# Optimization experiments

Measured on AMD Instinct MI355X. Metric: run time of the kernel, lower is better.

## Reference

```python
import jax, jax.numpy as jnp
import numpy as np

HIDDEN = 1024
HEADS = 16
HEAD_DIM = HIDDEN // HEADS  # 64
B, S = 2, 2048


def setup_inputs() -> dict:
    key = jax.random.key(0)
    ks = jax.random.split(key, 12)
    lim_h = 1.0 / np.sqrt(HEAD_DIM)
    lim_o = 1.0 / np.sqrt(HIDDEN)
    u = lambda k, shape, lim: jax.random.uniform(k, shape, jnp.float32, -lim, lim)
    return {
        "query": jax.random.normal(ks[0], (B, S, HIDDEN), jnp.float32),
        "key": jax.random.normal(ks[1], (B, S, HIDDEN), jnp.float32),
        "value": jax.random.normal(ks[2], (B, S, HIDDEN), jnp.float32),
        "mask": jax.random.randint(ks[3], (B, 1, S, S), 0, 2, jnp.int32),
        "Wq": u(ks[4], (HEAD_DIM, HEAD_DIM), lim_h), "bq": u(ks[5], (HEAD_DIM,), lim_h),
        "Wk": u(ks[6], (HEAD_DIM, HEAD_DIM), lim_h), "bk": u(ks[7], (HEAD_DIM,), lim_h),
        "Wv": u(ks[8], (HEAD_DIM, HEAD_DIM), lim_h), "bv": u(ks[9], (HEAD_DIM,), lim_h),
        "Wo": u(ks[10], (HIDDEN, HIDDEN), lim_o), "bo": u(ks[11], (HIDDEN,), lim_o),
    }


def reference(query, key, value, mask, Wq, bq, Wk, bk, Wv, bv, Wo, bo):
    b = query.shape[0]
    # view [B, S, H, D]; per-head linear is SHARED across heads (head_dim x head_dim)
    q = query.reshape(b, -1, HEADS, HEAD_DIM) @ Wq.T + bq
    k = key.reshape(b, -1, HEADS, HEAD_DIM) @ Wk.T + bk
    v = value.reshape(b, -1, HEADS, HEAD_DIM) @ Wv.T + bv
    scores = jnp.einsum('nqhd,nkhd->nhqk', q, k)  # [B, H, Sq, Sk]
    scores = jnp.where(mask == 0, jnp.float32(-1e20), scores)
    # NOTE: original scales by sqrt(hidden_dim), not sqrt(head_dim)
    attn = jax.nn.softmax(scores / np.sqrt(HIDDEN).astype(np.float32), axis=3)
    out = jnp.einsum('nhql,nlhd->nqhd', attn, v).reshape(b, query.shape[1], HIDDEN)
    return out @ Wo.T + bo
```

## Files before the change

kernel.cpp:

```cpp
#include <hip/hip_runtime.h>
#include <hip/hip_bf16.h>

#define NB 2
#define NS 2048
#define NH 16
#define ND 64
#define NHID 1024

#define QSCALE 0.045084220f

typedef __attribute__((ext_vector_type(8))) short bf16x8;
typedef __attribute__((ext_vector_type(4))) short s16x4;
typedef __attribute__((ext_vector_type(4))) float f32x4;

typedef __attribute__((address_space(3))) unsigned int lds_u32;
typedef __attribute__((address_space(1))) unsigned int glb_u32;

__device__ inline void gl_lds16(const void* g, void* l) {
  __builtin_amdgcn_global_load_lds((const glb_u32*)g, (lds_u32*)l, 16, 0, 0);
}

__device__ inline short f2bf(float f) {
  __hip_bfloat16 h = __float2bfloat16(f);
  short s; __builtin_memcpy(&s, &h, 2); return s;
}

__device__ inline bf16x8 cvt8(const float* __restrict__ p) {
  float4 x = *(const float4*)p;
  float4 y = *(const float4*)(p + 4);
  bf16x8 r;
  r[0] = f2bf(x.x); r[1] = f2bf(x.y); r[2] = f2bf(x.z); r[3] = f2bf(x.w);
  r[4] = f2bf(y.x); r[5] = f2bf(y.y); r[6] = f2bf(y.z); r[7] = f2bf(y.w);
  return r;
}

__global__ __launch_bounds__(256) void prep(
    const int* __restrict__ mask, unsigned* __restrict__ mp,
    const float* __restrict__ Wq, const float* __restrict__ Wk,
    const float* __restrict__ Wv, const float* __restrict__ Wo,
    short* __restrict__ Wq_b, short* __restrict__ Wk_b,
    short* __restrict__ Wv_b, short* __restrict__ Wo_b)
{
  if (blockIdx.x < 1024) {
    int idx = blockIdx.x * 256 + threadIdx.x;
    const int4* src = (const int4*)(mask + (long)idx * 32);
    unsigned w = 0;
#pragma unroll
    for (int i = 0; i < 8; ++i) {
      int4 v = src[i];
      w |= (v.x != 0 ? 1u : 0u) << (i * 4 + 0);
      w |= (v.y != 0 ? 1u : 0u) << (i * 4 + 1);
      w |= (v.z != 0 ? 1u : 0u) << (i * 4 + 2);
      w |= (v.w != 0 ? 1u : 0u) << (i * 4 + 3);
    }
    mp[idx] = w;
  } else {
    int i = ((blockIdx.x - 1024) * 256 + threadIdx.x) * 4;
    const float* src; short* dst; int off; float sc = 1.0f;
    if (i < 1048576)      { src = Wo; dst = Wo_b; off = i; }
    else {
      int j = i - 1048576;
      if (j < 4096)       { src = Wq; dst = Wq_b; off = j; sc = QSCALE; }
      else if (j < 8192)  { src = Wk; dst = Wk_b; off = j - 4096; }
      else                { src = Wv; dst = Wv_b; off = j - 8192; }
    }
    float4 v = *(const float4*)(src + off);
    s16x4 o;
    o[0] = f2bf(v.x * sc); o[1] = f2bf(v.y * sc);
    o[2] = f2bf(v.z * sc); o[3] = f2bf(v.w * sc);
    *(s16x4*)(dst + off) = o;
  }
}

__global__ __launch_bounds__(256) void qk_proj(
    const float* __restrict__ qin, const float* __restrict__ kin,
    const short* __restrict__ Wq_b, const float* __restrict__ bq,
    const short* __restrict__ Wk_b, const float* __restrict__ bk,
    short* __restrict__ Qws, short* __restrict__ Kws)
{
  __shared__ __align__(16) short ldsT[4][16][72];
  const int tid = threadIdx.x;
  const int w = tid >> 6, lane = tid & 63;
  const int c = lane & 15, qq = lane >> 4;
  const int t = blockIdx.x * 4 + w;
  const int b = t >> 11, s = t & (NS - 1);
  const int aoff = (t * 16 + c) * 64 + qq * 8;
  const int row0 = lane >> 3, inner = lane & 7;

#pragma unroll
  for (int m = 0; m < 2; ++m) {
    const float* X  = (m == 0) ? qin  : kin;
    const short* W  = (m == 0) ? Wq_b : Wk_b;
    const float* bb = (m == 0) ? bq   : bk;
    short* dst      = (m == 0) ? Qws  : Kws;
    const float bsc = (m == 0) ? QSCALE : 1.0f;

    bf16x8 a0 = cvt8(X + aoff);
    bf16x8 a1 = cvt8(X + aoff + 32);

#pragma unroll
    for (int nt = 0; nt < 4; ++nt) {
      f32x4 z = {0.f, 0.f, 0.f, 0.f};
      const short* wp = W + (nt * 16 + c) * 64 + qq * 8;
      bf16x8 b0 = *(const bf16x8*)(wp);
      bf16x8 b1 = *(const bf16x8*)(wp + 32);
      z = __builtin_amdgcn_mfma_f32_16x16x32_bf16(a0, b0, z, 0, 0, 0);
      z = __builtin_amdgcn_mfma_f32_16x16x32_bf16(a1, b1, z, 0, 0, 0);
      float bias = bb[nt * 16 + c] * bsc;
#pragma unroll
      for (int r = 0; r < 4; ++r)
        ldsT[w][qq * 4 + r][nt * 16 + c] = f2bf(z[r] + bias);
    }

    bf16x8 v0 = *(const bf16x8*)&ldsT[w][row0][inner * 8];
    bf16x8 v1 = *(const bf16x8*)&ldsT[w][row0 + 8][inner * 8];
    int bh0 = b * NH + row0, bh1 = b * NH + row0 + 8;
    *(bf16x8*)(dst + (bh0 * NS + s) * 64 + inner * 8) = v0;
    *(bf16x8*)(dst + (bh1 * NS + s) * 64 + inner * 8) = v1;
  }
}

__global__ __launch_bounds__(256) void vproj(
    const float* __restrict__ vin, const short* __restrict__ Wv_b,
    const float* __restrict__ bv, short* __restrict__ Vt)
{
  __shared__ __align__(16) short ldsVT[64][72];
  const int tid = threadIdx.x;
  const int g = tid >> 6, lane = tid & 63;
  const int c = lane & 15, qq = lane >> 4;
  const int bh = blockIdx.x >> 5;
  const int stile = blockIdx.x & 31;
  const int b = bh >> 4, h = bh & 15;
  const int sb = stile * 64;

  bf16x8 wv[8];
  float bias[4];
#pragma unroll
  for (int nt = 0; nt < 4; ++nt) {
    const short* wp = Wv_b + (nt * 16 + c) * 64 + qq * 8;
    wv[nt * 2]     = *(const bf16x8*)(wp);
    wv[nt * 2 + 1] = *(const bf16x8*)(wp + 32);
    bias[nt] = bv[nt * 16 + c];
  }

  const float* ap = vin + ((size_t)((b * NS + sb + 16 * g + c) * 16 + h)) * 64 + qq * 8;
  bf16x8 a0 = cvt8(ap);
  bf16x8 a1 = cvt8(ap + 32);
#pragma unroll
  for (int nt = 0; nt < 4; ++nt) {
    f32x4 z = {0.f, 0.f, 0.f, 0.f};
    z = __builtin_amdgcn_mfma_f32_16x16x32_bf16(a0, wv[nt * 2], z, 0, 0, 0);
    z = __builtin_amdgcn_mfma_f32_16x16x32_bf16(a1, wv[nt * 2 + 1], z, 0, 0, 0);
    ushort4 u;
    u.x = (unsigned short)f2bf(z[0] + bias[nt]);
    u.y = (unsigned short)f2bf(z[1] + bias[nt]);
    u.z = (unsigned short)f2bf(z[2] + bias[nt]);
    u.w = (unsigned short)f2bf(z[3] + bias[nt]);
    *(ushort4*)&ldsVT[nt * 16 + c][16 * g + qq * 4] = u;
  }
  __syncthreads();

#pragma unroll
  for (int j = 0; j < 2; ++j) {
    int idx = tid + 256 * j;
    int d = idx >> 3, unit = idx & 7;
    bf16x8 o = *(const bf16x8*)&ldsVT[d][unit * 8];
    *(bf16x8*)(Vt + ((size_t)(bh * 64 + d)) * NS + sb + unit * 8) = o;
  }
}

__global__ __launch_bounds__(256) void attn(
    const short* __restrict__ Qws, const short* __restrict__ Kws,
    const short* __restrict__ Vt, const unsigned* __restrict__ Mp,
    short* __restrict__ AO)
{
  __shared__ __align__(16) short Ks[2][64][64];
  __shared__ __align__(16) short Vs[2][64][64];
  __shared__ __align__(16) short Ps[4][32][72];

  const int tid = threadIdx.x;
  const int w = tid >> 6, lane = tid & 63;
  const int c = lane & 15, qq = lane >> 4;
  const int bh = blockIdx.x & 31;
  const int qtile = blockIdx.x >> 5;
  const int b = bh >> 4, h = bh & 15;
  const int qbase = qtile * 128 + w * 32;

  const short* Qp = Qws + (size_t)bh * (NS * 64);
  const short* Kp = Kws + (size_t)bh * (NS * 64);
  const short* Vp = Vt + (size_t)bh * (64 * NS);
  const unsigned* mrow = Mp + (size_t)b * (NS * (NS / 32));

  bf16x8 aq[2][2];
#pragma unroll
  for (int nq = 0; nq < 2; ++nq) {
    const short* qp = Qp + (qbase + nq * 16 + c) * 64 + qq * 8;
    aq[nq][0] = *(const bf16x8*)(qp);
    aq[nq][1] = *(const bf16x8*)(qp + 32);
  }

  float lsum[2] = {0.f, 0.f};
  f32x4 O[2][4];
#pragma unroll
  for (int nq = 0; nq < 2; ++nq)
#pragma unroll
    for (int dt = 0; dt < 4; ++dt) { f32x4 z = {0.f, 0.f, 0.f, 0.f}; O[nq][dt] = z; }

  const int srow = lane >> 3;
  const int sunit = (lane & 7) ^ srow;
  auto stage = [&](int kt, int buf) {
#pragma unroll
    for (int i = 0; i < 2; ++i) {
      int j = w * 2 + i;
      const short* gk = Kp + ((size_t)(kt * 64 + j * 8 + srow)) * 64 + sunit * 8;
      gl_lds16(gk, &Ks[buf][0][0] + j * 512);
      const short* gv = Vp + ((size_t)(j * 8 + srow)) * NS + kt * 64 + sunit * 8;
      gl_lds16(gv, &Vs[buf][0][0] + j * 512);
    }
  };

  stage(0, 0);
  __syncthreads();

  for (int kt = 0; kt < NS / 64; ++kt) {
    const int buf = kt & 1;
    if (kt < NS / 64 - 1) stage(kt + 1, buf ^ 1);

    uint2 mw[2];
#pragma unroll
    for (int nq = 0; nq < 2; ++nq)
      mw[nq] = *(const uint2*)(mrow +
          (size_t)(qbase + nq * 16 + c) * (NS / 32) + kt * 2);

    f32x4 st[4][2];
#pragma unroll
    for (int mt = 0; mt < 4; ++mt) {
      const short* kb = &Ks[buf][mt * 16 + c][0];
      bf16x8 ak0 = *(const bf16x8*)(kb + ((qq ^ (c & 7)) << 3));
      bf16x8 ak1 = *(const bf16x8*)(kb + (((4 + qq) ^ (c & 7)) << 3));
#pragma unroll
      for (int nq = 0; nq < 2; ++nq) {
        f32x4 z = {0.f, 0.f, 0.f, 0.f};
        z = __builtin_amdgcn_mfma_f32_16x16x32_bf16(ak0, aq[nq][0], z, 0, 0, 0);
        z = __builtin_amdgcn_mfma_f32_16x16x32_bf16(ak1, aq[nq][1], z, 0, 0, 0);
        st[mt][nq] = z;
      }
    }

#pragma unroll
    for (int mt = 0; mt < 4; ++mt) {
#pragma unroll
      for (int nq = 0; nq < 2; ++nq) {
        unsigned wsel = (mt & 2) ? mw[nq].y : mw[nq].x;
        unsigned nib = (wsel >> (((mt & 1) << 4) + (qq << 2))) & 0xFu;
        f32x4 s = st[mt][nq];
        float e0 = (nib & 1u) ? __builtin_amdgcn_exp2f(s[0]) : 0.f;
        float e1 = (nib & 2u) ? __builtin_amdgcn_exp2f(s[1]) : 0.f;
        float e2 = (nib & 4u) ? __builtin_amdgcn_exp2f(s[2]) : 0.f;
        float e3 = (nib & 8u) ? __builtin_amdgcn_exp2f(s[3]) : 0.f;
        lsum[nq] += (e0 + e1) + (e2 + e3);
        ushort4 u;
        u.x = (unsigned short)f2bf(e0);
        u.y = (unsigned short)f2bf(e1);
        u.z = (unsigned short)f2bf(e2);
        u.w = (unsigned short)f2bf(e3);
        *(ushort4*)&Ps[w][nq * 16 + c][mt * 16 + (qq << 2)] = u;
      }
    }

#pragma unroll
    for (int ks = 0; ks < 2; ++ks) {
      bf16x8 pf[2];
#pragma unroll
      for (int nq = 0; nq < 2; ++nq)
        pf[nq] = *(const bf16x8*)&Ps[w][nq * 16 + c][ks * 32 + qq * 8];
#pragma unroll
      for (int dt = 0; dt < 4; ++dt) {
        const short* vb = &Vs[buf][dt * 16 + c][0];
        bf16x8 vf = *(const bf16x8*)(vb + ((((ks << 2) + qq) ^ (c & 7)) << 3));
#pragma unroll
        for (int nq = 0; nq < 2; ++nq)
          O[nq][dt] = __builtin_amdgcn_mfma_f32_16x16x32_bf16(vf, pf[nq], O[nq][dt], 0, 0, 0);
      }
    }

    __syncthreads();
  }

#pragma unroll
  for (int nq = 0; nq < 2; ++nq) {
    float v = lsum[nq];
    v += __shfl_xor(v, 16);
    v += __shfl_xor(v, 32);
    lsum[nq] = 1.0f / fmaxf(v, 1e-30f);
  }

#pragma unroll
  for (int nq = 0; nq < 2; ++nq) {
    int row = qbase + nq * 16 + c;
#pragma unroll
    for (int dt = 0; dt < 4; ++dt) {
      ushort4 u;
      u.x = (unsigned short)f2bf(O[nq][dt][0] * lsum[nq]);
      u.y = (unsigned short)f2bf(O[nq][dt][1] * lsum[nq]);
      u.z = (unsigned short)f2bf(O[nq][dt][2] * lsum[nq]);
      u.w = (unsigned short)f2bf(O[nq][dt][3] * lsum[nq]);
      *(ushort4*)(AO + ((size_t)(b * NS + row)) * NHID + h * 64 + dt * 16 + qq * 4) = u;
    }
  }
}

__global__ __launch_bounds__(256, 2) void oproj(
    const short* __restrict__ X, const short* __restrict__ Wo_b,
    const float* __restrict__ bo, float* __restrict__ out)
{
  __shared__ __align__(16) short As[2][64][64];
  __shared__ __align__(16) short Bs[2][128][64];
  const int tid = threadIdx.x;
  const int w = tid >> 6, lane = tid & 63;
  const int c = lane & 15, qq = lane >> 4;
  const int rowbase = blockIdx.x * 64;
  const int colbase = blockIdx.y * 128;
  const int mh = w & 1, nh = w >> 1;

  const int srow = lane >> 3;
  const int sunit = (lane & 7) ^ srow;

  auto stage = [&](int kb, int buf) {
#pragma unroll
    for (int i = 0; i < 6; ++i) {
      int t = w * 6 + i;
      if (t < 8) {
        const short* g = X + (size_t)(rowbase + t * 8 + srow) * NHID
                           + kb * 64 + sunit * 8;
        gl_lds16(g, &As[buf][0][0] + t * 512);
      } else {
        int j = t - 8;
        const short* g = Wo_b + (size_t)(colbase + j * 8 + srow) * NHID
                              + kb * 64 + sunit * 8;
        gl_lds16(g, &Bs[buf][0][0] + j * 512);
      }
    }
  };

  f32x4 acc[2][4];
#pragma unroll
  for (int mt = 0; mt < 2; ++mt)
#pragma unroll
    for (int nt = 0; nt < 4; ++nt) { f32x4 z = {0.f, 0.f, 0.f, 0.f}; acc[mt][nt] = z; }

  stage(0, 0);
  __syncthreads();

  for (int kb = 0; kb < NHID / 64; ++kb) {
    const int buf = kb & 1;
    if (kb < NHID / 64 - 1) stage(kb + 1, buf ^ 1);

    bf16x8 af[2][2];
#pragma unroll
    for (int mt = 0; mt < 2; ++mt) {
      const short* ap = &As[buf][mh * 32 + mt * 16 + c][0];
#pragma unroll
      for (int ks = 0; ks < 2; ++ks)
        af[mt][ks] = *(const bf16x8*)(ap + ((((ks << 2) + qq) ^ (c & 7)) << 3));
    }
#pragma unroll
    for (int nt = 0; nt < 4; ++nt) {
      const short* bp = &Bs[buf][nh * 64 + nt * 16 + c][0];
#pragma unroll
      for (int ks = 0; ks < 2; ++ks) {
        bf16x8 bf = *(const bf16x8*)(bp + ((((ks << 2) + qq) ^ (c & 7)) << 3));
#pragma unroll
        for (int mt = 0; mt < 2; ++mt)
          acc[mt][nt] = __builtin_amdgcn_mfma_f32_16x16x32_bf16(af[mt][ks], bf, acc[mt][nt], 0, 0, 0);
      }
    }

    __syncthreads();
  }

#pragma unroll
  for (int nt = 0; nt < 4; ++nt) {
    int col = colbase + nh * 64 + nt * 16 + c;
    float bias = bo[col];
#pragma unroll
    for (int mt = 0; mt < 2; ++mt) {
      int row = rowbase + mh * 32 + mt * 16 + qq * 4;
#pragma unroll
      for (int r = 0; r < 4; ++r)
        out[(size_t)(row + r) * NHID + col] = acc[mt][nt][r] + bias;
    }
  }
}

extern "C" void kernel_launch(void* const* d_in, const int* in_sizes, int n_in,
                              void* d_out, int out_size, void* d_ws, size_t ws_size,
                              hipStream_t stream) {
  const float* qin = (const float*)d_in[0];
  const float* kin = (const float*)d_in[1];
  const float* vin = (const float*)d_in[2];
  const int*  mask = (const int*)d_in[3];
  const float* Wq = (const float*)d_in[4];
  const float* bq = (const float*)d_in[5];
  const float* Wk = (const float*)d_in[6];
  const float* bk = (const float*)d_in[7];
  const float* Wv = (const float*)d_in[8];
  const float* bv = (const float*)d_in[9];
  const float* Wo = (const float*)d_in[10];
  const float* bo = (const float*)d_in[11];
  float* out = (float*)d_out;

  char* ws = (char*)d_ws;
  short* Qws = (short*)(ws);
  short* Kws = (short*)(ws + (size_t)(8 << 20));
  short* Vt  = (short*)(ws + (size_t)(16 << 20));
  short* AO  = (short*)(ws + (size_t)(24 << 20));
  unsigned* Mp = (unsigned*)(ws + (size_t)(32 << 20));
  short* Wo_b = (short*)(ws + (size_t)(33 << 20));
  short* Wq_b = (short*)(ws + (size_t)(35 << 20));
  short* Wk_b = (short*)(ws + (size_t)(35 << 20) + 8192);
  short* Wv_b = (short*)(ws + (size_t)(35 << 20) + 16384);

  prep<<<2060, 256, 0, stream>>>(mask, Mp, Wq, Wk, Wv, Wo, Wq_b, Wk_b, Wv_b, Wo_b);
  qk_proj<<<NB * NS / 4, 256, 0, stream>>>(qin, kin, Wq_b, bq, Wk_b, bk, Qws, Kws);
  vproj<<<(NB * NH) * (NS / 64), 256, 0, stream>>>(vin, Wv_b, bv, Vt);
  attn<<<(NB * NH) * (NS / 128), 256, 0, stream>>>(Qws, Kws, Vt, Mp, AO);
  oproj<<<dim3(64, 8), 256, 0, stream>>>(AO, Wo_b, bo, out);
}
```

Measured before the change: 222.3 us.

## Use two waves with 64 query rows each and MFMA-based row sums

The attention kernel now runs 128 threads per block, and each wave owns 64 query rows instead of 32. This doubles reuse of every K/V fragment read from LDS per MFMA and halves the number of waves issuing LDS reads. The softmax denominator is now computed by an extra MFMA of the bf16 P tile against a vector of ones, replacing the scalar adds and cross-lane shuffles. The cost is higher register pressure from 16 O accumulators plus 4 sum accumulators, fewer waves per block to hide latency, and row sums taken from bf16-rounded probabilities.

```diff
diff --git a/kernel.cpp b/kernel.cpp
--- a/kernel.cpp
+++ b/kernel.cpp
@@ -169,14 +169,14 @@
   }
 }
 
-__global__ __launch_bounds__(256) void attn(
+__global__ __launch_bounds__(128) void attn(
     const short* __restrict__ Qws, const short* __restrict__ Kws,
     const short* __restrict__ Vt, const unsigned* __restrict__ Mp,
     short* __restrict__ AO)
 {
   __shared__ __align__(16) short Ks[2][64][64];
   __shared__ __align__(16) short Vs[2][64][64];
-  __shared__ __align__(16) short Ps[4][32][72];
+  __shared__ __align__(16) short Ps[2][64][72];
 
   const int tid = threadIdx.x;
   const int w = tid >> 6, lane = tid & 63;
@@ -184,34 +184,41 @@
   const int bh = blockIdx.x & 31;
   const int qtile = blockIdx.x >> 5;
   const int b = bh >> 4, h = bh & 15;
-  const int qbase = qtile * 128 + w * 32;
+  const int qbase = qtile * 128 + w * 64;
 
   const short* Qp = Qws + (size_t)bh * (NS * 64);
   const short* Kp = Kws + (size_t)bh * (NS * 64);
   const short* Vp = Vt + (size_t)bh * (64 * NS);
   const unsigned* mrow = Mp + (size_t)b * (NS * (NS / 32));
 
-  bf16x8 aq[2][2];
-#pragma unroll
-  for (int nq = 0; nq < 2; ++nq) {
+  bf16x8 aq[4][2];
+#pragma unroll
+  for (int nq = 0; nq < 4; ++nq) {
     const short* qp = Qp + (qbase + nq * 16 + c) * 64 + qq * 8;
     aq[nq][0] = *(const bf16x8*)(qp);
     aq[nq][1] = *(const bf16x8*)(qp + 32);
   }
 
-  float lsum[2] = {0.f, 0.f};
-  f32x4 O[2][4];
-#pragma unroll
-  for (int nq = 0; nq < 2; ++nq)
-#pragma unroll
-    for (int dt = 0; dt < 4; ++dt) { f32x4 z = {0.f, 0.f, 0.f, 0.f}; O[nq][dt] = z; }
+  bf16x8 ones;
+#pragma unroll
+  for (int i = 0; i < 8; ++i) ones[i] = (short)0x3F80;
+
+  const f32x4 ZV = {0.f, 0.f, 0.f, 0.f};
+  f32x4 O[4][4];
+  f32x4 Osum[4];
+#pragma unroll
+  for (int nq = 0; nq < 4; ++nq) {
+    Osum[nq] = ZV;
+#pragma unroll
+    for (int dt = 0; dt < 4; ++dt) O[nq][dt] = ZV;
+  }
 
   const int srow = lane >> 3;
   const int sunit = (lane & 7) ^ srow;
   auto stage = [&](int kt, int buf) {
 #pragma unroll
-    for (int i = 0; i < 2; ++i) {
-      int j = w * 2 + i;
+    for (int i = 0; i < 4; ++i) {
+      int j = w * 4 + i;
       const short* gk = Kp + ((size_t)(kt * 64 + j * 8 + srow)) * 64 + sunit * 8;
       gl_lds16(gk, &Ks[buf][0][0] + j * 512);
       const short* gv = Vp + ((size_t)(j * 8 + srow)) * NS + kt * 64 + sunit * 8;
@@ -226,39 +233,27 @@
     const int buf = kt & 1;
     if (kt < NS / 64 - 1) stage(kt + 1, buf ^ 1);
 
-    uint2 mw[2];
-#pragma unroll
-    for (int nq = 0; nq < 2; ++nq)
+    uint2 mw[4];
+#pragma unroll
+    for (int nq = 0; nq < 4; ++nq)
       mw[nq] = *(const uint2*)(mrow +
           (size_t)(qbase + nq * 16 + c) * (NS / 32) + kt * 2);
 
-    f32x4 st[4][2];
 #pragma unroll
     for (int mt = 0; mt < 4; ++mt) {
       const short* kb = &Ks[buf][mt * 16 + c][0];
       bf16x8 ak0 = *(const bf16x8*)(kb + ((qq ^ (c & 7)) << 3));
       bf16x8 ak1 = *(const bf16x8*)(kb + (((4 + qq) ^ (c & 7)) << 3));
 #pragma unroll
-      for (int nq = 0; nq < 2; ++nq) {
-        f32x4 z = {0.f, 0.f, 0.f, 0.f};
-        z = __builtin_amdgcn_mfma_f32_16x16x32_bf16(ak0, aq[nq][0], z, 0, 0, 0);
+      for (int nq = 0; nq < 4; ++nq) {
+        f32x4 z = __builtin_amdgcn_mfma_f32_16x16x32_bf16(ak0, aq[nq][0], ZV, 0, 0, 0);
         z = __builtin_amdgcn_mfma_f32_16x16x32_bf16(ak1, aq[nq][1], z, 0, 0, 0);
-        st[mt][nq] = z;
-      }
-    }
-
-#pragma unroll
-    for (int mt = 0; mt < 4; ++mt) {
-#pragma unroll
-      for (int nq = 0; nq < 2; ++nq) {
         unsigned wsel = (mt & 2) ? mw[nq].y : mw[nq].x;
         unsigned nib = (wsel >> (((mt & 1) << 4) + (qq << 2))) & 0xFu;
-        f32x4 s = st[mt][nq];
-        float e0 = (nib & 1u) ? __builtin_amdgcn_exp2f(s[0]) : 0.f;
-        float e1 = (nib & 2u) ? __builtin_amdgcn_exp2f(s[1]) : 0.f;
-        float e2 = (nib & 4u) ? __builtin_amdgcn_exp2f(s[2]) : 0.f;
-        float e3 = (nib & 8u) ? __builtin_amdgcn_exp2f(s[3]) : 0.f;
-        lsum[nq] += (e0 + e1) + (e2 + e3);
+        float e0 = (nib & 1u) ? __builtin_amdgcn_exp2f(z[0]) : 0.f;
+        float e1 = (nib & 2u) ? __builtin_amdgcn_exp2f(z[1]) : 0.f;
+        float e2 = (nib & 4u) ? __builtin_amdgcn_exp2f(z[2]) : 0.f;
+        float e3 = (nib & 8u) ? __builtin_amdgcn_exp2f(z[3]) : 0.f;
         ushort4 u;
         u.x = (unsigned short)f2bf(e0);
         u.y = (unsigned short)f2bf(e1);
@@ -270,16 +265,18 @@
 
 #pragma unroll
     for (int ks = 0; ks < 2; ++ks) {
-      bf16x8 pf[2];
-#pragma unroll
-      for (int nq = 0; nq < 2; ++nq)
+      bf16x8 pf[4];
+#pragma unroll
+      for (int nq = 0; nq < 4; ++nq) {
         pf[nq] = *(const bf16x8*)&Ps[w][nq * 16 + c][ks * 32 + qq * 8];
+        Osum[nq] = __builtin_amdgcn_mfma_f32_16x16x32_bf16(ones, pf[nq], Osum[nq], 0, 0, 0);
+      }
 #pragma unroll
       for (int dt = 0; dt < 4; ++dt) {
         const short* vb = &Vs[buf][dt * 16 + c][0];
         bf16x8 vf = *(const bf16x8*)(vb + ((((ks << 2) + qq) ^ (c & 7)) << 3));
 #pragma unroll
-        for (int nq = 0; nq < 2; ++nq)
+        for (int nq = 0; nq < 4; ++nq)
           O[nq][dt] = __builtin_amdgcn_mfma_f32_16x16x32_bf16(vf, pf[nq], O[nq][dt], 0, 0, 0);
       }
     }
@@ -288,23 +285,16 @@
   }
 
 #pragma unroll
-  for (int nq = 0; nq < 2; ++nq) {
-    float v = lsum[nq];
-    v += __shfl_xor(v, 16);
-    v += __shfl_xor(v, 32);
-    lsum[nq] = 1.0f / fmaxf(v, 1e-30f);
-  }
-
-#pragma unroll
-  for (int nq = 0; nq < 2; ++nq) {
+  for (int nq = 0; nq < 4; ++nq) {
+    float inv = 1.0f / fmaxf(Osum[nq][0], 1e-30f);
     int row = qbase + nq * 16 + c;
 #pragma unroll
     for (int dt = 0; dt < 4; ++dt) {
       ushort4 u;
-      u.x = (unsigned short)f2bf(O[nq][dt][0] * lsum[nq]);
-      u.y = (unsigned short)f2bf(O[nq][dt][1] * lsum[nq]);
-      u.z = (unsigned short)f2bf(O[nq][dt][2] * lsum[nq]);
-      u.w = (unsigned short)f2bf(O[nq][dt][3] * lsum[nq]);
+      u.x = (unsigned short)f2bf(O[nq][dt][0] * inv);
+      u.y = (unsigned short)f2bf(O[nq][dt][1] * inv);
+      u.z = (unsigned short)f2bf(O[nq][dt][2] * inv);
+      u.w = (unsigned short)f2bf(O[nq][dt][3] * inv);
       *(ushort4*)(AO + ((size_t)(b * NS + row)) * NHID + h * 64 + dt * 16 + qq * 4) = u;
     }
   }
@@ -424,6 +414,6 @@
   prep<<<2060, 256, 0, stream>>>(mask, Mp, Wq, Wk, Wv, Wo, Wq_b, Wk_b, Wv_b, Wo_b);
   qk_proj<<<NB * NS / 4, 256, 0, stream>>>(qin, kin, Wq_b, bq, Wk_b, bk, Qws, Kws);
   vproj<<<(NB * NH) * (NS / 64), 256, 0, stream>>>(vin, Wv_b, bv, Vt);
-  attn<<<(NB * NH) * (NS / 128), 256, 0, stream>>>(Qws, Kws, Vt, Mp, AO);
+  attn<<<(NB * NH) * (NS / 128), 128, 0, stream>>>(Qws, Kws, Vt, Mp, AO);
   oproj<<<dim3(64, 8), 256, 0, stream>>>(AO, Wo_b, bo, out);
 }
```

Result: slower. 245.6 us (+10.5%).

## Merge QK and V projections into one launch; MFMA row-sum and packed bf16 in attention

Applied to the files above, without the earlier changes.

Combines the separate QK and V projection kernels into one launch that dispatches on block index, removing a kernel launch and the gap between the two. In attention, the masked exp is now computed branch-free on a clamped input (-128 instead of skipping), and the softmax denominator comes from an extra MFMA against a ones vector instead of scalar adds plus cross-lane shuffles. Scores are consumed right after each QK MFMA instead of being held in a 4x2 register array, and bf16 conversions use packed two-element converts. The extra MFMA adds matrix-core work, and exp2(-128) leaves masked weights tiny but not exactly zero.

```diff
diff --git a/kernel.cpp b/kernel.cpp
--- a/kernel.cpp
+++ b/kernel.cpp
@@ -23,6 +23,12 @@
 __device__ inline short f2bf(float f) {
   __hip_bfloat16 h = __float2bfloat16(f);
   short s; __builtin_memcpy(&s, &h, 2); return s;
+}
+
+__device__ inline unsigned pk2bf(float a, float b) {
+  float2 t; t.x = a; t.y = b;
+  __hip_bfloat162 h = __float22bfloat162_rn(t);
+  unsigned u; __builtin_memcpy(&u, &h, 4); return u;
 }
 
 __device__ inline bf16x8 cvt8(const float* __restrict__ p) {
@@ -72,100 +78,97 @@
   }
 }
 
-__global__ __launch_bounds__(256) void qk_proj(
+__global__ __launch_bounds__(256) void qkv_proj(
     const float* __restrict__ qin, const float* __restrict__ kin,
+    const float* __restrict__ vin,
     const short* __restrict__ Wq_b, const float* __restrict__ bq,
     const short* __restrict__ Wk_b, const float* __restrict__ bk,
-    short* __restrict__ Qws, short* __restrict__ Kws)
+    const short* __restrict__ Wv_b, const float* __restrict__ bv,
+    short* __restrict__ Qws, short* __restrict__ Kws, short* __restrict__ Vt)
 {
   __shared__ __align__(16) short ldsT[4][16][72];
+  __shared__ __align__(16) short ldsVT[64][72];
   const int tid = threadIdx.x;
   const int w = tid >> 6, lane = tid & 63;
   const int c = lane & 15, qq = lane >> 4;
-  const int t = blockIdx.x * 4 + w;
-  const int b = t >> 11, s = t & (NS - 1);
-  const int aoff = (t * 16 + c) * 64 + qq * 8;
-  const int row0 = lane >> 3, inner = lane & 7;
-
-#pragma unroll
-  for (int m = 0; m < 2; ++m) {
-    const float* X  = (m == 0) ? qin  : kin;
-    const short* W  = (m == 0) ? Wq_b : Wk_b;
-    const float* bb = (m == 0) ? bq   : bk;
-    short* dst      = (m == 0) ? Qws  : Kws;
-    const float bsc = (m == 0) ? QSCALE : 1.0f;
-
-    bf16x8 a0 = cvt8(X + aoff);
-    bf16x8 a1 = cvt8(X + aoff + 32);
-
+
+  if (blockIdx.x < 1024) {
+    const int t = blockIdx.x * 4 + w;
+    const int b = t >> 11, s = t & (NS - 1);
+    const int aoff = (t * 16 + c) * 64 + qq * 8;
+    const int row0 = lane >> 3, inner = lane & 7;
+
+#pragma unroll
+    for (int m = 0; m < 2; ++m) {
+      const float* X  = (m == 0) ? qin  : kin;
+      const short* W  = (m == 0) ? Wq_b : Wk_b;
+      const float* bb = (m == 0) ? bq   : bk;
+      short* dst      = (m == 0) ? Qws  : Kws;
+      const float bsc = (m == 0) ? QSCALE : 1.0f;
+
+      bf16x8 a0 = cvt8(X + aoff);
+      bf16x8 a1 = cvt8(X + aoff + 32);
+
+#pragma unroll
+      for (int nt = 0; nt < 4; ++nt) {
+        f32x4 z = {0.f, 0.f, 0.f, 0.f};
+        const short* wp = W + (nt * 16 + c) * 64 + qq * 8;
+        bf16x8 b0 = *(const bf16x8*)(wp);
+        bf16x8 b1 = *(const bf16x8*)(wp + 32);
+        z = __builtin_amdgcn_mfma_f32_16x16x32_bf16(a0, b0, z, 0, 0, 0);
+        z = __builtin_amdgcn_mfma_f32_16x16x32_bf16(a1, b1, z, 0, 0, 0);
+        float bias = bb[nt * 16 + c] * bsc;
+#pragma unroll
+        for (int r = 0; r < 4; ++r)
+          ldsT[w][qq * 4 + r][nt * 16 + c] = f2bf(z[r] + bias);
+      }
+
+      bf16x8 v0 = *(const bf16x8*)&ldsT[w][row0][inner * 8];
+      bf16x8 v1 = *(const bf16x8*)&ldsT[w][row0 + 8][inner * 8];
+      int bh0 = b * NH + row0, bh1 = b * NH + row0 + 8;
+      *(bf16x8*)(dst + (bh0 * NS + s) * 64 + inner * 8) = v0;
+      *(bf16x8*)(dst + (bh1 * NS + s) * 64 + inner * 8) = v1;
+    }
+  } else {
+    const int bid = blockIdx.x - 1024;
+    const int g = w;
+    const int bh = bid >> 5;
+    const int stile = bid & 31;
+    const int b = bh >> 4, h = bh & 15;
+    const int sb = stile * 64;
+
+    bf16x8 wv[8];
+    float bias[4];
+#pragma unroll
+    for (int nt = 0; nt < 4; ++nt) {
+      const short* wp = Wv_b + (nt * 16 + c) * 64 + qq * 8;
+      wv[nt * 2]     = *(const bf16x8*)(wp);
+      wv[nt * 2 + 1] = *(const bf16x8*)(wp + 32);
+      bias[nt] = bv[nt * 16 + c];
+    }
+
+    const float* ap = vin + ((size_t)((b * NS + sb + 16 * g + c) * 16 + h)) * 64 + qq * 8;
+    bf16x8 a0 = cvt8(ap);
+    bf16x8 a1 = cvt8(ap + 32);
 #pragma unroll
     for (int nt = 0; nt < 4; ++nt) {
       f32x4 z = {0.f, 0.f, 0.f, 0.f};
-      const short* wp = W + (nt * 16 + c) * 64 + qq * 8;
-      bf16x8 b0 = *(const bf16x8*)(wp);
-      bf16x8 b1 = *(const bf16x8*)(wp + 32);
-      z = __builtin_amdgcn_mfma_f32_16x16x32_bf16(a0, b0, z, 0, 0, 0);
-      z = __builtin_amdgcn_mfma_f32_16x16x32_bf16(a1, b1, z, 0, 0, 0);
-      float bias = bb[nt * 16 + c] * bsc;
-#pragma unroll
-      for (int r = 0; r < 4; ++r)
-        ldsT[w][qq * 4 + r][nt * 16 + c] = f2bf(z[r] + bias);
-    }
-
-    bf16x8 v0 = *(const bf16x8*)&ldsT[w][row0][inner * 8];
-    bf16x8 v1 = *(const bf16x8*)&ldsT[w][row0 + 8][inner * 8];
-    int bh0 = b * NH + row0, bh1 = b * NH + row0 + 8;
-    *(bf16x8*)(dst + (bh0 * NS + s) * 64 + inner * 8) = v0;
-    *(bf16x8*)(dst + (bh1 * NS + s) * 64 + inner * 8) = v1;
-  }
-}
-
-__global__ __launch_bounds__(256) void vproj(
-    const float* __restrict__ vin, const short* __restrict__ Wv_b,
-    const float* __restrict__ bv, short* __restrict__ Vt)
-{
-  __shared__ __align__(16) short ldsVT[64][72];
-  const int tid = threadIdx.x;
-  const int g = tid >> 6, lane = tid & 63;
-  const int c = lane & 15, qq = lane >> 4;
-  const int bh = blockIdx.x >> 5;
-  const int stile = blockIdx.x & 31;
-  const int b = bh >> 4, h = bh & 15;
-  const int sb = stile * 64;
-
-  bf16x8 wv[8];
-  float bias[4];
-#pragma unroll
-  for (int nt = 0; nt < 4; ++nt) {
-    const short* wp = Wv_b + (nt * 16 + c) * 64 + qq * 8;
-    wv[nt * 2]     = *(const bf16x8*)(wp);
-    wv[nt * 2 + 1] = *(const bf16x8*)(wp + 32);
-    bias[nt] = bv[nt * 16 + c];
-  }
-
-  const float* ap = vin + ((size_t)((b * NS + sb + 16 * g + c) * 16 + h)) * 64 + qq * 8;
-  bf16x8 a0 = cvt8(ap);
-  bf16x8 a1 = cvt8(ap + 32);
-#pragma unroll
-  for (int nt = 0; nt < 4; ++nt) {
-    f32x4 z = {0.f, 0.f, 0.f, 0.f};
-    z = __builtin_amdgcn_mfma_f32_16x16x32_bf16(a0, wv[nt * 2], z, 0, 0, 0);
-    z = __builtin_amdgcn_mfma_f32_16x16x32_bf16(a1, wv[nt * 2 + 1], z, 0, 0, 0);
-    ushort4 u;
-    u.x = (unsigned short)f2bf(z[0] + bias[nt]);
-    u.y = (unsigned short)f2bf(z[1] + bias[nt]);
-    u.z = (unsigned short)f2bf(z[2] + bias[nt]);
-    u.w = (unsigned short)f2bf(z[3] + bias[nt]);
-    *(ushort4*)&ldsVT[nt * 16 + c][16 * g + qq * 4] = u;
-  }
-  __syncthreads();
-
-#pragma unroll
-  for (int j = 0; j < 2; ++j) {
-    int idx = tid + 256 * j;
-    int d = idx >> 3, unit = idx & 7;
-    bf16x8 o = *(const bf16x8*)&ldsVT[d][unit * 8];
-    *(bf16x8*)(Vt + ((size_t)(bh * 64 + d)) * NS + sb + unit * 8) = o;
+      z = __builtin_amdgcn_mfma_f32_16x16x32_bf16(a0, wv[nt * 2], z, 0, 0, 0);
+      z = __builtin_amdgcn_mfma_f32_16x16x32_bf16(a1, wv[nt * 2 + 1], z, 0, 0, 0);
+      uint2 u;
+      u.x = pk2bf(z[0] + bias[nt], z[1] + bias[nt]);
+      u.y = pk2bf(z[2] + bias[nt], z[3] + bias[nt]);
+      *(uint2*)&ldsVT[nt * 16 + c][16 * g + qq * 4] = u;
+    }
+    __syncthreads();
+
+#pragma unroll
+    for (int j = 0; j < 2; ++j) {
+      int idx = tid + 256 * j;
+      int d = idx >> 3, unit = idx & 7;
+      bf16x8 o = *(const bf16x8*)&ldsVT[d][unit * 8];
+      *(bf16x8*)(Vt + ((size_t)(bh * 64 + d)) * NS + sb + unit * 8) = o;
+    }
   }
 }
 
@@ -199,12 +202,19 @@
     aq[nq][1] = *(const bf16x8*)(qp + 32);
   }
 
-  float lsum[2] = {0.f, 0.f};
+  bf16x8 ones;
+#pragma unroll
+  for (int i = 0; i < 8; ++i) ones[i] = (short)0x3F80;
+
+  const f32x4 ZV = {0.f, 0.f, 0.f, 0.f};
   f32x4 O[2][4];
-#pragma unroll
-  for (int nq = 0; nq < 2; ++nq)
-#pragma unroll
-    for (int dt = 0; dt < 4; ++dt) { f32x4 z = {0.f, 0.f, 0.f, 0.f}; O[nq][dt] = z; }
+  f32x4 Osum[2];
+#pragma unroll
+  for (int nq = 0; nq < 2; ++nq) {
+    Osum[nq] = ZV;
+#pragma unroll
+    for (int dt = 0; dt < 4; ++dt) O[nq][dt] = ZV;
+  }
 
   const int srow = lane >> 3;
   const int sunit = (lane & 7) ^ srow;
@@ -232,7 +242,6 @@
       mw[nq] = *(const uint2*)(mrow +
           (size_t)(qbase + nq * 16 + c) * (NS / 32) + kt * 2);
 
-    f32x4 st[4][2];
 #pragma unroll
     for (int mt = 0; mt < 4; ++mt) {
       const short* kb = &Ks[buf][mt * 16 + c][0];
@@ -240,31 +249,18 @@
       bf16x8 ak1 = *(const bf16x8*)(kb + (((4 + qq) ^ (c & 7)) << 3));
 #pragma unroll
       for (int nq = 0; nq < 2; ++nq) {
-        f32x4 z = {0.f, 0.f, 0.f, 0.f};
-        z = __builtin_amdgcn_mfma_f32_16x16x32_bf16(ak0, aq[nq][0], z, 0, 0, 0);
+        f32x4 z = __builtin_amdgcn_mfma_f32_16x16x32_bf16(ak0, aq[nq][0], ZV, 0, 0, 0);
         z = __builtin_amdgcn_mfma_f32_16x16x32_bf16(ak1, aq[nq][1], z, 0, 0, 0);
-        st[mt][nq] = z;
-      }
-    }
-
-#pragma unroll
-    for (int mt = 0; mt < 4; ++mt) {
-#pragma unroll
-      for (int nq = 0; nq < 2; ++nq) {
         unsigned wsel = (mt & 2) ? mw[nq].y : mw[nq].x;
         unsigned nib = (wsel >> (((mt & 1) << 4) + (qq << 2))) & 0xFu;
-        f32x4 s = st[mt][nq];
-        float e0 = (nib & 1u) ? __builtin_amdgcn_exp2f(s[0]) : 0.f;
-        float e1 = (nib & 2u) ? __builtin_amdgcn_exp2f(s[1]) : 0.f;
-        float e2 = (nib & 4u) ? __builtin_amdgcn_exp2f(s[2]) : 0.f;
-        float e3 = (nib & 8u) ? __builtin_amdgcn_exp2f(s[3]) : 0.f;
-        lsum[nq] += (e0 + e1) + (e2 + e3);
-        ushort4 u;
-        u.x = (unsigned short)f2bf(e0);
-        u.y = (unsigned short)f2bf(e1);
-        u.z = (unsigned short)f2bf(e2);
-        u.w = (unsigned short)f2bf(e3);
-        *(ushort4*)&Ps[w][nq * 16 + c][mt * 16 + (qq << 2)] = u;
+        float e0 = __builtin_amdgcn_exp2f((nib & 1u) ? z[0] : -128.f);
+        float e1 = __builtin_amdgcn_exp2f((nib & 2u) ? z[1] : -128.f);
+        float e2 = __builtin_amdgcn_exp2f((nib & 4u) ? z[2] : -128.f);
+        float e3 = __builtin_amdgcn_exp2f((nib & 8u) ? z[3] : -128.f);
+        uint2 u;
+        u.x = pk2bf(e0, e1);
+        u.y = pk2bf(e2, e3);
+        *(uint2*)&Ps[w][nq * 16 + c][mt * 16 + (qq << 2)] = u;
       }
     }
 
@@ -272,8 +268,10 @@
     for (int ks = 0; ks < 2; ++ks) {
       bf16x8 pf[2];
 #pragma unroll
-      for (int nq = 0; nq < 2; ++nq)
+      for (int nq = 0; nq < 2; ++nq) {
         pf[nq] = *(const bf16x8*)&Ps[w][nq * 16 + c][ks * 32 + qq * 8];
+        Osum[nq] = __builtin_amdgcn_mfma_f32_16x16x32_bf16(ones, pf[nq], Osum[nq], 0, 0, 0);
+      }
 #pragma unroll
       for (int dt = 0; dt < 4; ++dt) {
         const short* vb = &Vs[buf][dt * 16 + c][0];
@@ -289,23 +287,14 @@
 
 #pragma unroll
   for (int nq = 0; nq < 2; ++nq) {
-    float v = lsum[nq];
-    v += __shfl_xor(v, 16);
-    v += __shfl_xor(v, 32);
-    lsum[nq] = 1.0f / fmaxf(v, 1e-30f);
-  }
-
-#pragma unroll
-  for (int nq = 0; nq < 2; ++nq) {
+    float inv = 1.0f / fmaxf(Osum[nq][0], 1e-30f);
     int row = qbase + nq * 16 + c;
 #pragma unroll
     for (int dt = 0; dt < 4; ++dt) {
-      ushort4 u;
-      u.x = (unsigned short)f2bf(O[nq][dt][0] * lsum[nq]);
-      u.y = (unsigned short)f2bf(O[nq][dt][1] * lsum[nq]);
-      u.z = (unsigned short)f2bf(O[nq][dt][2] * lsum[nq]);
-      u.w = (unsigned short)f2bf(O[nq][dt][3] * lsum[nq]);
-      *(ushort4*)(AO + ((size_t)(b * NS + row)) * NHID + h * 64 + dt * 16 + qq * 4) = u;
+      uint2 u;
+      u.x = pk2bf(O[nq][dt][0] * inv, O[nq][dt][1] * inv);
+      u.y = pk2bf(O[nq][dt][2] * inv, O[nq][dt][3] * inv);
+      *(uint2*)(AO + ((size_t)(b * NS + row)) * NHID + h * 64 + dt * 16 + qq * 4) = u;
     }
   }
 }
@@ -422,8 +411,8 @@
   short* Wv_b = (short*)(ws + (size_t)(35 << 20) + 16384);
 
   prep<<<2060, 256, 0, stream>>>(mask, Mp, Wq, Wk, Wv, Wo, Wq_b, Wk_b, Wv_b, Wo_b);
-  qk_proj<<<NB * NS / 4, 256, 0, stream>>>(qin, kin, Wq_b, bq, Wk_b, bk, Qws, Kws);
-  vproj<<<(NB * NH) * (NS / 64), 256, 0, stream>>>(vin, Wv_b, bv, Vt);
+  qkv_proj<<<2048, 256, 0, stream>>>(qin, kin, vin, Wq_b, bq, Wk_b, bk, Wv_b, bv,
+                                     Qws, Kws, Vt);
   attn<<<(NB * NH) * (NS / 128), 256, 0, stream>>>(Qws, Kws, Vt, Mp, AO);
   oproj<<<dim3(64, 8), 256, 0, stream>>>(AO, Wo_b, bo, out);
 }
```

Measured after the change: 222.5 us. Within noise of the previous version (+0.1%).
